# Performance work log

Measured on AMD Instinct MI355X. Metric: run time of the kernel, lower is better.

Reference implementation:

```python
import jax, jax.numpy as jnp
import numpy as np

MODEL_DIM = 1024
NUM_HEADS = 16
HEAD_DIM = MODEL_DIM // NUM_HEADS
WINDOW = 4


def local_mask(seq_len):
    i = jnp.arange(seq_len)
    return jnp.abs(i[:, None] - i[None, :]) <= WINDOW  # [S,S] bool


def setup_inputs() -> dict:
    key = jax.random.key(0)
    ks = jax.random.split(key, 9)
    d = MODEL_DIM
    s = 0.02
    return {
        "x": jax.random.normal(ks[0], (4, 2048, d), dtype=jnp.float32),
        "Wq": jax.random.normal(ks[1], (d, d), dtype=jnp.float32) * s,
        "bq": jnp.zeros((d,), dtype=jnp.float32),
        "Wk": jax.random.normal(ks[2], (d, d), dtype=jnp.float32) * s,
        "bk": jnp.zeros((d,), dtype=jnp.float32),
        "Wv": jax.random.normal(ks[3], (d, d), dtype=jnp.float32) * s,
        "bv": jnp.zeros((d,), dtype=jnp.float32),
        "Wo": jax.random.normal(ks[4], (d, d), dtype=jnp.float32) * s,
        "bo": jnp.zeros((d,), dtype=jnp.float32),
    }


def reference(x, Wq, bq, Wk, bk, Wv, bv, Wo, bo):
    B, S, D = x.shape
    H, Hd = NUM_HEADS, HEAD_DIM
    # linear projections (torch Linear: x @ W.T + b; here W stored pre-transposed)
    q = (x @ Wq + bq).reshape(B, S, H, Hd).transpose(0, 2, 1, 3)  # [B,H,S,Hd]
    k = (x @ Wk + bk).reshape(B, S, H, Hd).transpose(0, 2, 1, 3)
    v = (x @ Wv + bv).reshape(B, S, H, Hd).transpose(0, 2, 1, 3)
    scores = jnp.einsum("bhqd,bhkd->bhqk", q, k) / jnp.sqrt(jnp.float32(Hd))
    mask = local_mask(S)[None, None]  # [1,1,S,S]
    scores = jnp.where(mask, scores, -jnp.inf)
    weights = jax.nn.softmax(scores, axis=-1)  # [B,H,S,S]
    out = jnp.einsum("bhqk,bhkd->bhqd", weights, v)
    out = out.transpose(0, 2, 1, 3).reshape(B, S, D)
    out = out @ Wo + bo
    return (out, weights)
```

## Files before the change

kernel.cpp:

```cpp
#include <hip/hip_runtime.h>


typedef __attribute__((ext_vector_type(8))) short short8;
typedef __attribute__((ext_vector_type(4))) float f32x4;

#define B_    4
#define S_    2048
#define D_    1024
#define H_    16
#define HD_   64
#define WIN_  4
#define NROW  (B_ * S_)
#define OUT0_ELEMS  ((size_t)B_ * S_ * D_)
#define WEIGHT_ELEMS ((size_t)B_ * H_ * S_ * S_)

__device__ __forceinline__ unsigned short f2bf(float f) {
  unsigned int u = __float_as_uint(f);
  u += 0x7fffu + ((u >> 16) & 1u);
  return (unsigned short)(u >> 16);
}

__global__ __launch_bounds__(256) void xconv_k(const float* __restrict__ x,
                                               unsigned short* __restrict__ o) {
  int i = blockIdx.x * 256 + threadIdx.x;
  float4 f = reinterpret_cast<const float4*>(x)[i];
  ushort4 u;
  u.x = f2bf(f.x); u.y = f2bf(f.y); u.z = f2bf(f.z); u.w = f2bf(f.w);
  reinterpret_cast<ushort4*>(o)[i] = u;
}

__global__ __launch_bounds__(256) void wconv_k(const float* __restrict__ W0,
                                               const float* __restrict__ W1,
                                               const float* __restrict__ W2,
                                               const float* __restrict__ W3,
                                               unsigned short* __restrict__ out) {
  __shared__ float t[32][33];
  const float* Ws[4] = {W0, W1, W2, W3};
  const float* W = Ws[blockIdx.z];
  unsigned short* o = out + (size_t)blockIdx.z * D_ * D_;
  int tx = threadIdx.x;
  int ty = threadIdx.y;
  int n0 = blockIdx.x * 32, k0 = blockIdx.y * 32;
#pragma unroll
  for (int i = 0; i < 4; ++i)
    t[ty + 8 * i][tx] = W[(size_t)(k0 + ty + 8 * i) * D_ + (n0 + tx)];
  __syncthreads();
#pragma unroll
  for (int i = 0; i < 4; ++i)
    o[(size_t)(n0 + ty + 8 * i) * D_ + (k0 + tx)] = f2bf(t[tx][ty + 8 * i]);
}

#define GLD16(g, l)                                                            \
  __builtin_amdgcn_global_load_lds(                                            \
      (const __attribute__((address_space(1))) unsigned int*)(g),              \
      (__attribute__((address_space(3))) unsigned int*)(l), 16, 0, 0)

template <int MODE>
__global__ __launch_bounds__(256) void gemm_bf16_k(
    const unsigned short* __restrict__ A, const unsigned short* __restrict__ WtBase,
    const float* __restrict__ b0, const float* __restrict__ b1,
    const float* __restrict__ b2, float* __restrict__ o0, float* __restrict__ o1,
    float* __restrict__ o2) {
  __shared__ unsigned short As[128 * 32];
  __shared__ unsigned short Bs[128 * 32];
  const int z = blockIdx.z;
  const unsigned short* Bt = WtBase + (size_t)z * (D_ * D_);
  const float* bias = (z == 0) ? b0 : (z == 1) ? b1 : b2;
  float* outp = (z == 0) ? o0 : (z == 1) ? o1 : o2;

  const int tid = threadIdx.x;
  const int lane = tid & 63;
  const int wid = tid >> 6;
  const int wm = wid >> 1, wn = wid & 1;
  const int row0 = blockIdx.x * 128;
  const int col0 = blockIdx.y * 128;

  f32x4 acc[4][4] = {};

  const int frow = lane & 15;
  const int koff = (lane >> 4) << 3;

  for (int kt = 0; kt < D_; kt += 32) {
#pragma unroll
    for (int i = 0; i < 2; ++i) {
      int c = tid + (i << 8);
      int r = c >> 2;
      int kk = (c & 3) << 3;
      GLD16(A + (size_t)(row0 + r) * D_ + kt + kk, (char*)As + c * 16);
      GLD16(Bt + (size_t)(col0 + r) * D_ + kt + kk, (char*)Bs + c * 16);
    }
    __syncthreads();
    short8 af[4], bfr[4];
#pragma unroll
    for (int mi = 0; mi < 4; ++mi)
      af[mi] = *reinterpret_cast<const short8*>(
          &As[(wm * 64 + mi * 16 + frow) * 32 + koff]);
#pragma unroll
    for (int ni = 0; ni < 4; ++ni)
      bfr[ni] = *reinterpret_cast<const short8*>(
          &Bs[(wn * 64 + ni * 16 + frow) * 32 + koff]);
#pragma unroll
    for (int mi = 0; mi < 4; ++mi)
#pragma unroll
      for (int ni = 0; ni < 4; ++ni)
        acc[mi][ni] = __builtin_amdgcn_mfma_f32_16x16x32_bf16(
            af[mi], bfr[ni], acc[mi][ni], 0, 0, 0);
    __syncthreads();
  }

#pragma unroll
  for (int mi = 0; mi < 4; ++mi) {
#pragma unroll
    for (int ni = 0; ni < 4; ++ni) {
#pragma unroll
      for (int r = 0; r < 4; ++r) {
        int gr = row0 + wm * 64 + mi * 16 + ((lane >> 4) << 2) + r;
        int gc = col0 + wn * 64 + ni * 16 + (lane & 15);
        float val = acc[mi][ni][r] + bias[gc];
        if (MODE == 0) {
          int b = gr >> 11, s = gr & (S_ - 1);
          int h = gc >> 6, hd = gc & 63;
          outp[(((size_t)(b * H_ + h) * S_ + s) << 6) + hd] = val;
        } else {
          outp[(size_t)gr * D_ + gc] = val;
        }
      }
    }
  }
}

__global__ __launch_bounds__(256) void attn_k(const float* __restrict__ Q,
                                              const float* __restrict__ K,
                                              const float* __restrict__ V,
                                              float* __restrict__ wout,
                                              unsigned short* __restrict__ attn) {
  int lane = threadIdx.x & 63;
  int wid = threadIdx.x >> 6;
  int row = blockIdx.x * 4 + wid;
  int s = row & (S_ - 1);
  int bh = row >> 11;
  int b = bh >> 4, h = bh & 15;
  float qd = Q[(size_t)row * HD_ + lane];
  const float* Kb = K + (size_t)bh * S_ * HD_;
  const float* Vb = V + (size_t)bh * S_ * HD_;

  float sc[9];
#pragma unroll
  for (int j = 0; j < 9; ++j) {
    int ks = s - WIN_ + j;
    bool ok = (ks >= 0) && (ks < S_);
    float v = ok ? qd * Kb[(size_t)ks * HD_ + lane] : 0.f;
#pragma unroll
    for (int off = 32; off > 0; off >>= 1) v += __shfl_xor(v, off, 64);
    sc[j] = ok ? v * 0.125f : -INFINITY;
  }
  float m = sc[0];
#pragma unroll
  for (int j = 1; j < 9; ++j) m = fmaxf(m, sc[j]);
  float w[9];
  float sum = 0.f;
#pragma unroll
  for (int j = 0; j < 9; ++j) { w[j] = __expf(sc[j] - m); sum += w[j]; }
  float inv = 1.f / sum;
#pragma unroll
  for (int j = 0; j < 9; ++j) w[j] *= inv;

  float o = 0.f;
#pragma unroll
  for (int j = 0; j < 9; ++j) {
    int ks = s - WIN_ + j;
    if (ks >= 0 && ks < S_) o += w[j] * Vb[(size_t)ks * HD_ + lane];
  }
  attn[((size_t)(b * S_ + s)) * D_ + h * HD_ + lane] = f2bf(o);

  f32x4* rowp = reinterpret_cast<f32x4*>(wout + (size_t)row * S_);
  const int lo = s - WIN_;
  const int hi = s + WIN_;
#pragma unroll
  for (int i = 0; i < 8; ++i) {
    int f = lane + (i << 6);
    int c0 = f << 2;
    f32x4 v4 = {0.f, 0.f, 0.f, 0.f};
    if (c0 + 3 >= lo && c0 <= hi) {
#pragma unroll
      for (int e = 0; e < 4; ++e) {
        int d = c0 + e - lo;
        float val = 0.f;
#pragma unroll
        for (int j = 0; j < 9; ++j)
          if (d == j) val = w[j];
        v4[e] = val;
      }
    }
    __builtin_nontemporal_store(v4, rowp + f);
  }
}

extern "C" void kernel_launch(void* const* d_in, const int* in_sizes, int n_in,
                              void* d_out, int out_size, void* d_ws,
                              size_t ws_size, hipStream_t stream) {
  const float* x = (const float*)d_in[0];
  const float* Wq = (const float*)d_in[1];
  const float* bq = (const float*)d_in[2];
  const float* Wk = (const float*)d_in[3];
  const float* bk = (const float*)d_in[4];
  const float* Wv = (const float*)d_in[5];
  const float* bv = (const float*)d_in[6];
  const float* Wo = (const float*)d_in[7];
  const float* bo = (const float*)d_in[8];
  float* out = (float*)d_out;
  float* wout = out + OUT0_ELEMS;

  char* ws = (char*)d_ws;
  unsigned short* x_bf = (unsigned short*)(ws);
  unsigned short* Wt = (unsigned short*)(ws + (16ull << 20));
  float* Qf = (float*)(ws + (24ull << 20));
  float* Kf = (float*)(ws + (56ull << 20));
  float* Vf = (float*)(ws + (88ull << 20));
  unsigned short* attn = (unsigned short*)(ws + (120ull << 20));

  xconv_k<<<NROW * D_ / 1024, 256, 0, stream>>>(x, x_bf);
  wconv_k<<<dim3(32, 32, 4), dim3(32, 8), 0, stream>>>(Wq, Wk, Wv, Wo, Wt);
  gemm_bf16_k<0><<<dim3(64, 8, 3), 256, 0, stream>>>(x_bf, Wt, bq, bk, bv, Qf,
                                                     Kf, Vf);
  attn_k<<<(B_ * H_ * S_) / 4, 256, 0, stream>>>(Qf, Kf, Vf, wout, attn);
  gemm_bf16_k<1><<<dim3(64, 8, 1), 256, 0, stream>>>(
      attn, Wt + (size_t)3 * D_ * D_, bo, bo, bo, out, out, out);
}
```

Before: 301.8 us.

## Spread zero-fill of attention weights across GEMM kernels and store QKV in bf16

The zero part of the dense 1 GB attention-weight output is now written in chunks from inside the QKV projection GEMM, the output projection GEMM and the attention kernel. This lets the memory-bound zero stores overlap with MFMA compute rather than running as one store-bound pass. The attention kernel itself now writes only the few nonzero window vectors per row. Q, K and V are also stored as bf16 instead of fp32, halving intermediate traffic at some cost in precision.

```diff
diff --git a/kernel.cpp b/kernel.cpp
--- a/kernel.cpp
+++ b/kernel.cpp
@@ -12,12 +12,32 @@
 #define WIN_  4
 #define NROW  (B_ * S_)
 #define OUT0_ELEMS  ((size_t)B_ * S_ * D_)
-#define WEIGHT_ELEMS ((size_t)B_ * H_ * S_ * S_)
+#define WROWS (B_ * H_ * S_)
+#define TOTAL_CH (67108864ull)
+#define Z0_CH 37748736ull
+#define Z1_CH 16777216ull
+#define ZA_BASE (Z0_CH + Z1_CH)
 
 __device__ __forceinline__ unsigned short f2bf(float f) {
   unsigned int u = __float_as_uint(f);
   u += 0x7fffu + ((u >> 16) & 1u);
   return (unsigned short)(u >> 16);
+}
+__device__ __forceinline__ float bf2f(unsigned short u) {
+  return __uint_as_float(((unsigned int)u) << 16);
+}
+
+__device__ __forceinline__ void zstore(f32x4* __restrict__ woutv, size_t g) {
+  int row = (int)(g >> 9);
+  int f = (int)(g & 511);
+  int s = row & (S_ - 1);
+  int f0 = (s > WIN_) ? ((s - WIN_) >> 2) : 0;
+  int hi = (s + WIN_ < S_ - 1) ? (s + WIN_) : (S_ - 1);
+  int f1 = hi >> 2;
+  if (f < f0 || f > f1) {
+    f32x4 z = {0.f, 0.f, 0.f, 0.f};
+    __builtin_nontemporal_store(z, woutv + g);
+  }
 }
 
 __global__ __launch_bounds__(256) void xconv_k(const float* __restrict__ x,
@@ -55,40 +75,39 @@
       (const __attribute__((address_space(1))) unsigned int*)(g),              \
       (__attribute__((address_space(3))) unsigned int*)(l), 16, 0, 0)
 
-template <int MODE>
-__global__ __launch_bounds__(256) void gemm_bf16_k(
-    const unsigned short* __restrict__ A, const unsigned short* __restrict__ WtBase,
-    const float* __restrict__ b0, const float* __restrict__ b1,
-    const float* __restrict__ b2, float* __restrict__ o0, float* __restrict__ o1,
-    float* __restrict__ o2) {
+__global__ __launch_bounds__(256) void gemm_qkv_k(
+    const unsigned short* __restrict__ A, const unsigned short* __restrict__ Wt,
+    const float* __restrict__ bq, const float* __restrict__ bk,
+    const float* __restrict__ bv, unsigned short* __restrict__ Qb,
+    unsigned short* __restrict__ Kb, unsigned short* __restrict__ Vb,
+    float* __restrict__ wout) {
   __shared__ unsigned short As[128 * 32];
   __shared__ unsigned short Bs[128 * 32];
-  const int z = blockIdx.z;
-  const unsigned short* Bt = WtBase + (size_t)z * (D_ * D_);
-  const float* bias = (z == 0) ? b0 : (z == 1) ? b1 : b2;
-  float* outp = (z == 0) ? o0 : (z == 1) ? o1 : o2;
-
   const int tid = threadIdx.x;
   const int lane = tid & 63;
   const int wid = tid >> 6;
   const int wm = wid >> 1, wn = wid & 1;
   const int row0 = blockIdx.x * 128;
   const int col0 = blockIdx.y * 128;
+  f32x4* woutv = (f32x4*)wout;
+  const unsigned int gt = (blockIdx.y * 64u + blockIdx.x) * 256u + tid;
 
   f32x4 acc[4][4] = {};
-
   const int frow = lane & 15;
   const int koff = (lane >> 4) << 3;
 
-  for (int kt = 0; kt < D_; kt += 32) {
+  for (int kt = 0; kt < 32; ++kt) {
 #pragma unroll
     for (int i = 0; i < 2; ++i) {
       int c = tid + (i << 8);
       int r = c >> 2;
       int kk = (c & 3) << 3;
-      GLD16(A + (size_t)(row0 + r) * D_ + kt + kk, (char*)As + c * 16);
-      GLD16(Bt + (size_t)(col0 + r) * D_ + kt + kk, (char*)Bs + c * 16);
-    }
+      GLD16(A + (size_t)(row0 + r) * D_ + (kt << 5) + kk, (char*)As + c * 16);
+      GLD16(Wt + (size_t)(col0 + r) * D_ + (kt << 5) + kk, (char*)Bs + c * 16);
+    }
+#pragma unroll
+    for (int j = 0; j < 3; ++j)
+      zstore(woutv, (size_t)(kt * 3 + j) * 393216u + gt);
     __syncthreads();
     short8 af[4], bfr[4];
 #pragma unroll
@@ -116,22 +135,86 @@
       for (int r = 0; r < 4; ++r) {
         int gr = row0 + wm * 64 + mi * 16 + ((lane >> 4) << 2) + r;
         int gc = col0 + wn * 64 + ni * 16 + (lane & 15);
-        float val = acc[mi][ni][r] + bias[gc];
-        if (MODE == 0) {
-          int b = gr >> 11, s = gr & (S_ - 1);
-          int h = gc >> 6, hd = gc & 63;
-          outp[(((size_t)(b * H_ + h) * S_ + s) << 6) + hd] = val;
-        } else {
-          outp[(size_t)gr * D_ + gc] = val;
-        }
+        int z = gc >> 10;
+        int ci = gc & 1023;
+        float bias = (z == 0) ? bq[ci] : (z == 1) ? bk[ci] : bv[ci];
+        unsigned short* outp = (z == 0) ? Qb : (z == 1) ? Kb : Vb;
+        int b = gr >> 11, s = gr & (S_ - 1);
+        int h = ci >> 6, hd = ci & 63;
+        outp[(((size_t)(b * H_ + h) * S_ + s) << 6) + hd] =
+            f2bf(acc[mi][ni][r] + bias);
       }
     }
   }
 }
 
-__global__ __launch_bounds__(256) void attn_k(const float* __restrict__ Q,
-                                              const float* __restrict__ K,
-                                              const float* __restrict__ V,
+__global__ __launch_bounds__(256) void gemm_out_k(
+    const unsigned short* __restrict__ A, const unsigned short* __restrict__ Bt,
+    const float* __restrict__ bias, float* __restrict__ o,
+    float* __restrict__ wout) {
+  __shared__ unsigned short As[128 * 32];
+  __shared__ unsigned short Bs[128 * 32];
+  const int tid = threadIdx.x;
+  const int lane = tid & 63;
+  const int wid = tid >> 6;
+  const int wm = wid >> 1, wn = wid & 1;
+  const int row0 = blockIdx.x * 128;
+  const int col0 = blockIdx.y * 128;
+  f32x4* woutv = (f32x4*)wout;
+  const unsigned int gt = (blockIdx.y * 64u + blockIdx.x) * 256u + tid;
+
+  f32x4 acc[4][4] = {};
+  const int frow = lane & 15;
+  const int koff = (lane >> 4) << 3;
+
+  for (int kt = 0; kt < 32; ++kt) {
+#pragma unroll
+    for (int i = 0; i < 2; ++i) {
+      int c = tid + (i << 8);
+      int r = c >> 2;
+      int kk = (c & 3) << 3;
+      GLD16(A + (size_t)(row0 + r) * D_ + (kt << 5) + kk, (char*)As + c * 16);
+      GLD16(Bt + (size_t)(col0 + r) * D_ + (kt << 5) + kk, (char*)Bs + c * 16);
+    }
+#pragma unroll
+    for (int j = 0; j < 4; ++j)
+      zstore(woutv, Z0_CH + (size_t)(kt * 4 + j) * 131072u + gt);
+    __syncthreads();
+    short8 af[4], bfr[4];
+#pragma unroll
+    for (int mi = 0; mi < 4; ++mi)
+      af[mi] = *reinterpret_cast<const short8*>(
+          &As[(wm * 64 + mi * 16 + frow) * 32 + koff]);
+#pragma unroll
+    for (int ni = 0; ni < 4; ++ni)
+      bfr[ni] = *reinterpret_cast<const short8*>(
+          &Bs[(wn * 64 + ni * 16 + frow) * 32 + koff]);
+#pragma unroll
+    for (int mi = 0; mi < 4; ++mi)
+#pragma unroll
+      for (int ni = 0; ni < 4; ++ni)
+        acc[mi][ni] = __builtin_amdgcn_mfma_f32_16x16x32_bf16(
+            af[mi], bfr[ni], acc[mi][ni], 0, 0, 0);
+    __syncthreads();
+  }
+
+#pragma unroll
+  for (int mi = 0; mi < 4; ++mi) {
+#pragma unroll
+    for (int ni = 0; ni < 4; ++ni) {
+#pragma unroll
+      for (int r = 0; r < 4; ++r) {
+        int gr = row0 + wm * 64 + mi * 16 + ((lane >> 4) << 2) + r;
+        int gc = col0 + wn * 64 + ni * 16 + (lane & 15);
+        o[(size_t)gr * D_ + gc] = acc[mi][ni][r] + bias[gc];
+      }
+    }
+  }
+}
+
+__global__ __launch_bounds__(256) void attn_k(const unsigned short* __restrict__ Q,
+                                              const unsigned short* __restrict__ K,
+                                              const unsigned short* __restrict__ V,
                                               float* __restrict__ wout,
                                               unsigned short* __restrict__ attn) {
   int lane = threadIdx.x & 63;
@@ -140,16 +223,16 @@
   int s = row & (S_ - 1);
   int bh = row >> 11;
   int b = bh >> 4, h = bh & 15;
-  float qd = Q[(size_t)row * HD_ + lane];
-  const float* Kb = K + (size_t)bh * S_ * HD_;
-  const float* Vb = V + (size_t)bh * S_ * HD_;
+  float qd = bf2f(Q[(size_t)row * HD_ + lane]);
+  const unsigned short* Kb = K + (size_t)bh * S_ * HD_;
+  const unsigned short* Vb = V + (size_t)bh * S_ * HD_;
 
   float sc[9];
 #pragma unroll
   for (int j = 0; j < 9; ++j) {
     int ks = s - WIN_ + j;
     bool ok = (ks >= 0) && (ks < S_);
-    float v = ok ? qd * Kb[(size_t)ks * HD_ + lane] : 0.f;
+    float v = ok ? qd * bf2f(Kb[(size_t)ks * HD_ + lane]) : 0.f;
 #pragma unroll
     for (int off = 32; off > 0; off >>= 1) v += __shfl_xor(v, off, 64);
     sc[j] = ok ? v * 0.125f : -INFINITY;
@@ -169,30 +252,34 @@
 #pragma unroll
   for (int j = 0; j < 9; ++j) {
     int ks = s - WIN_ + j;
-    if (ks >= 0 && ks < S_) o += w[j] * Vb[(size_t)ks * HD_ + lane];
+    if (ks >= 0 && ks < S_) o += w[j] * bf2f(Vb[(size_t)ks * HD_ + lane]);
   }
   attn[((size_t)(b * S_ + s)) * D_ + h * HD_ + lane] = f2bf(o);
 
+  const int lo = s - WIN_;
+  const int hiq = (s + WIN_ < S_ - 1) ? (s + WIN_) : (S_ - 1);
+  const int f0 = (s > WIN_) ? ((s - WIN_) >> 2) : 0;
+  const int f1 = hiq >> 2;
   f32x4* rowp = reinterpret_cast<f32x4*>(wout + (size_t)row * S_);
-  const int lo = s - WIN_;
-  const int hi = s + WIN_;
-#pragma unroll
-  for (int i = 0; i < 8; ++i) {
-    int f = lane + (i << 6);
-    int c0 = f << 2;
-    f32x4 v4 = {0.f, 0.f, 0.f, 0.f};
-    if (c0 + 3 >= lo && c0 <= hi) {
-#pragma unroll
-      for (int e = 0; e < 4; ++e) {
-        int d = c0 + e - lo;
-        float val = 0.f;
-#pragma unroll
-        for (int j = 0; j < 9; ++j)
-          if (d == j) val = w[j];
-        v4[e] = val;
-      }
-    }
-    __builtin_nontemporal_store(v4, rowp + f);
+  if (lane <= f1 - f0) {
+    f32x4 v4;
+#pragma unroll
+    for (int e = 0; e < 4; ++e) {
+      int d = ((f0 + lane) << 2) + e - lo;
+      float val = 0.f;
+#pragma unroll
+      for (int j = 0; j < 9; ++j)
+        if (d == j) val = w[j];
+      v4[e] = val;
+    }
+    __builtin_nontemporal_store(v4, rowp + f0 + lane);
+  }
+
+  unsigned int gtid = blockIdx.x * 256u + threadIdx.x;
+#pragma unroll
+  for (int k2 = 0; k2 < 2; ++k2) {
+    size_t g = ZA_BASE + (size_t)k2 * 8388608u + gtid;
+    if (g < TOTAL_CH) zstore((f32x4*)wout, g);
   }
 }
 
@@ -214,16 +301,16 @@
   char* ws = (char*)d_ws;
   unsigned short* x_bf = (unsigned short*)(ws);
   unsigned short* Wt = (unsigned short*)(ws + (16ull << 20));
-  float* Qf = (float*)(ws + (24ull << 20));
-  float* Kf = (float*)(ws + (56ull << 20));
-  float* Vf = (float*)(ws + (88ull << 20));
-  unsigned short* attn = (unsigned short*)(ws + (120ull << 20));
+  unsigned short* Qb = (unsigned short*)(ws + (24ull << 20));
+  unsigned short* Kb = (unsigned short*)(ws + (40ull << 20));
+  unsigned short* Vb = (unsigned short*)(ws + (56ull << 20));
+  unsigned short* attn = (unsigned short*)(ws + (72ull << 20));
 
   xconv_k<<<NROW * D_ / 1024, 256, 0, stream>>>(x, x_bf);
   wconv_k<<<dim3(32, 32, 4), dim3(32, 8), 0, stream>>>(Wq, Wk, Wv, Wo, Wt);
-  gemm_bf16_k<0><<<dim3(64, 8, 3), 256, 0, stream>>>(x_bf, Wt, bq, bk, bv, Qf,
-                                                     Kf, Vf);
-  attn_k<<<(B_ * H_ * S_) / 4, 256, 0, stream>>>(Qf, Kf, Vf, wout, attn);
-  gemm_bf16_k<1><<<dim3(64, 8, 1), 256, 0, stream>>>(
-      attn, Wt + (size_t)3 * D_ * D_, bo, bo, bo, out, out, out);
-}
+  gemm_qkv_k<<<dim3(64, 24), 256, 0, stream>>>(x_bf, Wt, bq, bk, bv, Qb, Kb,
+                                               Vb, wout);
+  attn_k<<<(B_ * H_ * S_) / 4, 256, 0, stream>>>(Qb, Kb, Vb, wout, attn);
+  gemm_out_k<<<dim3(64, 8), 256, 0, stream>>>(
+      attn, Wt + (size_t)3 * D_ * D_, bo, out, wout);
+}
```

Result: slower. 340.9 us (+12.9%).
